# Kernel tuning notes

Hardware: AMD Instinct MI355X
Metric: run time of the kernel (lower is better)

## Reference

```python
import jax, jax.numpy as jnp
import numpy as np


def setup_inputs() -> dict:
    key = jax.random.key(0)
    k1, k2 = jax.random.split(key)
    B, N, F = 16, 4096, 512
    S, K = 8, 1024          # splits, symbols per codebook
    D = F // S              # sub-vector dim
    x = jax.random.normal(k1, (B, N, F), dtype=jnp.float32)
    # torch init: uniform(-1/symbols, 1/symbols)
    codebooks = jax.random.uniform(k2, (S, K, D), dtype=jnp.float32,
                                   minval=-1.0 / K, maxval=1.0 / K)
    return {"x": x, "codebooks": codebooks}


def reference(x, codebooks):
    B, N, F = x.shape
    S, K, D = codebooks.shape
    xs = x.reshape(B, N, S, D)                       # split into S chunks
    x2 = jnp.sum(xs * xs, axis=-1, keepdims=True)    # [B,N,S,1]
    c2 = jnp.sum(codebooks * codebooks, axis=-1)     # [S,K]
    xc = jnp.einsum('bnsd,skd->bnsk', xs, codebooks)
    dist = x2 + c2[None, None] - 2.0 * xc            # [B,N,S,K]
    idx = jnp.argmin(dist, axis=-1)                  # [B,N,S]
    # gather chosen code vectors per split -> [B,N,S,D]
    sym = codebooks[jnp.arange(S)[None, None, :], idx]
    sg = jax.lax.stop_gradient
    # straight-through quantized output
    quant = (xs + sg(sym - xs)).reshape(B, N, F)
    # per-split mse (mean over B,N,D of each chunk), summed over splits
    dev = (jnp.sum(jnp.mean((sym - sg(xs)) ** 2, axis=(0, 1, 3)))
           + 0.25 * jnp.sum(jnp.mean((xs - sg(sym)) ** 2, axis=(0, 1, 3))))
    return quant, dev
```

## Files before the change

### kernel.cpp

```cpp
#include <hip/hip_runtime.h>
#include <cstdint>

constexpr int Bv = 16, Nv = 4096, Fv = 512, Sv = 8, Kv = 1024, Dv = 64;
constexpr int Mv = Bv * Nv;
#define BDIM 256
constexpr int RG = 4;

using bf16x8 = __attribute__((ext_vector_type(8))) short;
using f32x4  = __attribute__((ext_vector_type(4))) float;
typedef unsigned short u16;
typedef unsigned int u32;

__device__ __forceinline__ u16 bf16rne(float f) {
  union { float f; u32 u; } v; v.f = f;
  u32 u = v.u + 0x7FFFu + ((v.u >> 16) & 1u);
  return (u16)(u >> 16);
}

__device__ __forceinline__ void gload_lds16(const void* g, void* lds) {
  __builtin_amdgcn_global_load_lds(
      (const __attribute__((address_space(1))) void*)g,
      (__attribute__((address_space(3))) void*)lds, 16, 0, 0);
}

__global__ void prep_kernel(const float* __restrict__ cb, u16* __restrict__ swz,
                            float* __restrict__ c2m) {
  int idx = blockIdx.x * BDIM + threadIdx.x;
  int cw = idx & (Kv - 1);
  const float4* src = (const float4*)(cb + (size_t)idx * Dv);
  float v[64];
  float s2 = 0.f;
#pragma unroll
  for (int i = 0; i < 16; ++i) {
    float4 f = src[i];
    v[i * 4 + 0] = f.x; v[i * 4 + 1] = f.y; v[i * 4 + 2] = f.z; v[i * 4 + 3] = f.w;
    s2 += f.x * f.x + f.y * f.y + f.z * f.z + f.w * f.w;
  }
  c2m[idx] = -0.5f * s2;
  uint4* out = (uint4*)(swz + (size_t)idx * Dv);
#pragma unroll
  for (int slot = 0; slot < 8; ++slot) {
    int slotp = slot ^ (cw & 7);
    u32 w[4];
#pragma unroll
    for (int p = 0; p < 4; ++p)
      w[p] = (u32)bf16rne(v[slot * 8 + p * 2]) | ((u32)bf16rne(v[slot * 8 + p * 2 + 1]) << 16);
    uint4 pk; pk.x = w[0]; pk.y = w[1]; pk.z = w[2]; pk.w = w[3];
    out[slotp] = pk;
  }
}

__global__ __launch_bounds__(BDIM, 4) void pq_mfma(
    const float* __restrict__ x, const float* __restrict__ cb,
    const u16* __restrict__ swz, const float* __restrict__ c2m_g,
    float* __restrict__ quant, float* __restrict__ devpart) {
  __shared__ __attribute__((aligned(16))) u16 ring[4][3][32 * Dv];
  __shared__ __attribute__((aligned(16))) float c2_lds[Kv];

  const int tid = threadIdx.x;
  const int s = blockIdx.y;
  const int row0 = blockIdx.x * 256;
  const int wave = tid >> 6, lane = tid & 63;
  const int l15 = lane & 15, lg = lane >> 4;
  const int slotp0 = lg ^ (l15 & 7);
  const int slotp1 = (4 + lg) ^ (l15 & 7);

  const u16* swz_s = swz + (size_t)s * Kv * Dv;

  auto stage = [&](int t, int slot) {
    const u16* src = swz_s + (size_t)t * (32 * Dv) + lane * 8;
    u16* dst = &ring[wave][slot][0];
#pragma unroll
    for (int it = 0; it < 4; ++it)
      gload_lds16(src + it * 512, dst + it * 512);
  };

  gload_lds16(c2m_g + s * Kv + tid * 4, &c2_lds[(tid & ~63) * 4]);
  stage(0, 0); stage(1, 1);

  bf16x8 xf[RG][2];
  float x2p[RG];
#pragma unroll
  for (int rg = 0; rg < RG; ++rg) {
    x2p[rg] = 0.f;
    const int row = row0 + wave * 64 + rg * 16 + l15;
    const float* xp = x + (size_t)row * Fv + s * Dv + lg * 8;
#pragma unroll
    for (int h = 0; h < 2; ++h) {
      float4 f0 = *(const float4*)(xp + h * 32);
      float4 f1 = *(const float4*)(xp + h * 32 + 4);
      x2p[rg] += f0.x * f0.x + f0.y * f0.y + f0.z * f0.z + f0.w * f0.w
               + f1.x * f1.x + f1.y * f1.y + f1.z * f1.z + f1.w * f1.w;
      bf16x8 v;
      v[0] = (short)bf16rne(f0.x); v[1] = (short)bf16rne(f0.y);
      v[2] = (short)bf16rne(f0.z); v[3] = (short)bf16rne(f0.w);
      v[4] = (short)bf16rne(f1.x); v[5] = (short)bf16rne(f1.y);
      v[6] = (short)bf16rne(f1.z); v[7] = (short)bf16rne(f1.w);
      xf[rg][h] = v;
    }
  }

  float bv[RG];
#pragma unroll
  for (int rg = 0; rg < RG; ++rg) bv[rg] = -3.0e38f;

  asm volatile("s_waitcnt vmcnt(8)" ::: "memory");
  __builtin_amdgcn_s_barrier();

  auto tile = [&](int t, int slot) {
    const u16* base = &ring[wave][slot][0];
    bf16x8 a00 = *(const bf16x8*)(base + l15 * Dv + slotp0 * 8);
    bf16x8 a01 = *(const bf16x8*)(base + l15 * Dv + slotp1 * 8);
    bf16x8 a10 = *(const bf16x8*)(base + (16 + l15) * Dv + slotp0 * 8);
    bf16x8 a11 = *(const bf16x8*)(base + (16 + l15) * Dv + slotp1 * 8);
    f32x4 c2v0 = *(const f32x4*)&c2_lds[t * 32 + lg * 4];
    f32x4 c2v1 = *(const f32x4*)&c2_lds[t * 32 + 16 + lg * 4];
    const u32 kb0 = (u32)(t * 32) | (u32)(lg * 4);
    const u32 kb1 = kb0 | 16u;
    __builtin_amdgcn_s_setprio(1);
#pragma unroll
    for (int rg = 0; rg < RG; ++rg) {
      f32x4 acc = __builtin_amdgcn_mfma_f32_16x16x32_bf16(a00, xf[rg][0], c2v0, 0, 0, 0);
      acc = __builtin_amdgcn_mfma_f32_16x16x32_bf16(a01, xf[rg][1], acc, 0, 0, 0);
      f32x4 acd = __builtin_amdgcn_mfma_f32_16x16x32_bf16(a10, xf[rg][0], c2v1, 0, 0, 0);
      acd = __builtin_amdgcn_mfma_f32_16x16x32_bf16(a11, xf[rg][1], acd, 0, 0, 0);
      float p0 = __builtin_bit_cast(float, __builtin_bit_cast(u32, acc[0]) | kb0);
      float p1 = __builtin_bit_cast(float, __builtin_bit_cast(u32, acc[1]) | (kb0 | 1u));
      float p2 = __builtin_bit_cast(float, __builtin_bit_cast(u32, acc[2]) | (kb0 | 2u));
      float p3 = __builtin_bit_cast(float, __builtin_bit_cast(u32, acc[3]) | (kb0 | 3u));
      float q0 = __builtin_bit_cast(float, __builtin_bit_cast(u32, acd[0]) | kb1);
      float q1 = __builtin_bit_cast(float, __builtin_bit_cast(u32, acd[1]) | (kb1 | 1u));
      float q2 = __builtin_bit_cast(float, __builtin_bit_cast(u32, acd[2]) | (kb1 | 2u));
      float q3 = __builtin_bit_cast(float, __builtin_bit_cast(u32, acd[3]) | (kb1 | 3u));
      float m0 = fmaxf(fmaxf(p0, p1), p2);
      float m1 = fmaxf(fmaxf(p3, q0), q1);
      float m2 = fmaxf(fmaxf(q2, q3), bv[rg]);
      bv[rg] = fmaxf(fmaxf(m0, m1), m2);
    }
    __builtin_amdgcn_s_setprio(0);
  };

#pragma unroll 1
  for (int b = 0; b < 30; b += 3) {
    stage(b + 2, 2);
    asm volatile("s_waitcnt vmcnt(8)" ::: "memory");
    tile(b, 0);
    stage(b + 3, 0);
    asm volatile("s_waitcnt vmcnt(8)" ::: "memory");
    tile(b + 1, 1);
    stage(b + 4, 1);
    asm volatile("s_waitcnt vmcnt(8)" ::: "memory");
    tile(b + 2, 2);
  }
  asm volatile("s_waitcnt vmcnt(4)" ::: "memory");
  tile(30, 0);
  asm volatile("s_waitcnt vmcnt(0)" ::: "memory");
  tile(31, 1);

#pragma unroll
  for (int rg = 0; rg < RG; ++rg) {
    float b = bv[rg], xx = x2p[rg];
    b = fmaxf(b, __shfl_xor(b, 16, 64)); xx += __shfl_xor(xx, 16, 64);
    b = fmaxf(b, __shfl_xor(b, 32, 64)); xx += __shfl_xor(xx, 32, 64);
    bv[rg] = b; x2p[rg] = xx;
  }

  float dev = 0.f;
#pragma unroll
  for (int rg = 0; rg < RG; ++rg) dev += x2p[rg] - 2.f * bv[rg];
#pragma unroll
  for (int m = 1; m <= 8; m <<= 1) dev += __shfl_xor(dev, m, 64);
  if (lane == 0)
    devpart[((size_t)blockIdx.y * gridDim.x + blockIdx.x) * 4 + wave] = dev;

  const float* cbs = cb + (size_t)s * Kv * Dv;
  float* qbase = quant + (size_t)(row0 + wave * 64) * Fv + s * Dv;
#pragma unroll
  for (int i = 0; i < 16; ++i) {
    int rl = i * 4 + lg;
    int kk = __shfl(__builtin_bit_cast(int, bv[i >> 2]), 4 * (i & 3) + lg, 64) & 1023;
    f32x4 v = *(const f32x4*)(cbs + (size_t)kk * Dv + l15 * 4);
    __builtin_nontemporal_store(v, (f32x4*)(qbase + (size_t)rl * Fv + l15 * 4));
  }
}

__global__ void dev_reduce(const float* __restrict__ part, float* __restrict__ out) {
  __shared__ float sred[256];
  int tid = threadIdx.x;
  float s = 0.f;
  for (int i = tid; i < 8192; i += 256) s += part[i];
  sred[tid] = s;
  __syncthreads();
  for (int off = 128; off > 0; off >>= 1) {
    if (tid < off) sred[tid] += sred[tid + off];
    __syncthreads();
  }
  if (tid == 0) out[0] = sred[0] * (1.25f / 4194304.0f);
}

extern "C" void kernel_launch(void* const* d_in, const int* in_sizes, int n_in,
                              void* d_out, int out_size, void* d_ws, size_t ws_size,
                              hipStream_t stream) {
  const float* x = (const float*)d_in[0];
  const float* cb = (const float*)d_in[1];
  float* quant = (float*)d_out;
  float* dev = quant + (size_t)Mv * Fv;

  u16* swz = (u16*)d_ws;
  float* c2m = (float*)(swz + (size_t)Sv * Kv * Dv);
  float* part = c2m + Sv * Kv;

  prep_kernel<<<(Sv * Kv) / BDIM, BDIM, 0, stream>>>(cb, swz, c2m);
  dim3 grid(Mv / 256, Sv);
  pq_mfma<<<grid, BDIM, 0, stream>>>(x, cb, swz, c2m, quant, part);
  dev_reduce<<<1, 256, 0, stream>>>(part, dev);
}
```

Baseline: 116.7 us.

## Shrink LDS ring to 16-code tiles with register double-buffered fragment reads

After: 126.1 us. 1.08x slower.

```diff
diff --git a/kernel.cpp b/kernel.cpp
--- a/kernel.cpp
+++ b/kernel.cpp
@@ -54,7 +54,7 @@
     const float* __restrict__ x, const float* __restrict__ cb,
     const u16* __restrict__ swz, const float* __restrict__ c2m_g,
     float* __restrict__ quant, float* __restrict__ devpart) {
-  __shared__ __attribute__((aligned(16))) u16 ring[4][3][32 * Dv];
+  __shared__ __attribute__((aligned(16))) u16 ring[4][2][16 * Dv];
   __shared__ __attribute__((aligned(16))) float c2_lds[Kv];
 
   const int tid = threadIdx.x;
@@ -66,17 +66,17 @@
   const int slotp1 = (4 + lg) ^ (l15 & 7);
 
   const u16* swz_s = swz + (size_t)s * Kv * Dv;
-
-  auto stage = [&](int t, int slot) {
-    const u16* src = swz_s + (size_t)t * (32 * Dv) + lane * 8;
-    u16* dst = &ring[wave][slot][0];
-#pragma unroll
-    for (int it = 0; it < 4; ++it)
-      gload_lds16(src + it * 512, dst + it * 512);
+  u16* slot0 = &ring[wave][0][0];
+  u16* slot1 = &ring[wave][1][0];
+
+  auto stage = [&](int t, u16* dst) {
+    const u16* src = swz_s + (size_t)t * (16 * Dv) + lane * 8;
+    gload_lds16(src, dst);
+    gload_lds16(src + 512, dst + 512);
   };
 
   gload_lds16(c2m_g + s * Kv + tid * 4, &c2_lds[(tid & ~63) * 4]);
-  stage(0, 0); stage(1, 1);
+  stage(0, slot0); stage(1, slot1);
 
   bf16x8 xf[RG][2];
   float x2p[RG];
@@ -104,58 +104,82 @@
 #pragma unroll
   for (int rg = 0; rg < RG; ++rg) bv[rg] = -3.0e38f;
 
-  asm volatile("s_waitcnt vmcnt(8)" ::: "memory");
+  asm volatile("s_waitcnt vmcnt(2)" ::: "memory");
   __builtin_amdgcn_s_barrier();
 
-  auto tile = [&](int t, int slot) {
-    const u16* base = &ring[wave][slot][0];
-    bf16x8 a00 = *(const bf16x8*)(base + l15 * Dv + slotp0 * 8);
-    bf16x8 a01 = *(const bf16x8*)(base + l15 * Dv + slotp1 * 8);
-    bf16x8 a10 = *(const bf16x8*)(base + (16 + l15) * Dv + slotp0 * 8);
-    bf16x8 a11 = *(const bf16x8*)(base + (16 + l15) * Dv + slotp1 * 8);
-    f32x4 c2v0 = *(const f32x4*)&c2_lds[t * 32 + lg * 4];
-    f32x4 c2v1 = *(const f32x4*)&c2_lds[t * 32 + 16 + lg * 4];
-    const u32 kb0 = (u32)(t * 32) | (u32)(lg * 4);
-    const u32 kb1 = kb0 | 16u;
+  const u16* r0s0 = slot0 + l15 * Dv + slotp0 * 8;
+  const u16* r1s0 = slot0 + l15 * Dv + slotp1 * 8;
+  const u16* r0s1 = slot1 + l15 * Dv + slotp0 * 8;
+  const u16* r1s1 = slot1 + l15 * Dv + slotp1 * 8;
+
+  bf16x8 aE0, aE1, aO0, aO1;
+  f32x4 c2E, c2O;
+
+  aE0 = *(const bf16x8*)r0s0;
+  aE1 = *(const bf16x8*)r1s0;
+  c2E = *(const f32x4*)&c2_lds[lg * 4];
+
+  auto readO = [&](int t1) {
+    aO0 = *(const bf16x8*)r0s1;
+    aO1 = *(const bf16x8*)r1s1;
+    c2O = *(const f32x4*)&c2_lds[t1 * 16 + lg * 4];
+  };
+  auto readE = [&](int t1) {
+    aE0 = *(const bf16x8*)r0s0;
+    aE1 = *(const bf16x8*)r1s0;
+    c2E = *(const f32x4*)&c2_lds[t1 * 16 + lg * 4];
+  };
+  auto computeE = [&](int t) {
+    const u32 kb = (u32)(t * 16) | (u32)(lg * 4);
     __builtin_amdgcn_s_setprio(1);
 #pragma unroll
     for (int rg = 0; rg < RG; ++rg) {
-      f32x4 acc = __builtin_amdgcn_mfma_f32_16x16x32_bf16(a00, xf[rg][0], c2v0, 0, 0, 0);
-      acc = __builtin_amdgcn_mfma_f32_16x16x32_bf16(a01, xf[rg][1], acc, 0, 0, 0);
-      f32x4 acd = __builtin_amdgcn_mfma_f32_16x16x32_bf16(a10, xf[rg][0], c2v1, 0, 0, 0);
-      acd = __builtin_amdgcn_mfma_f32_16x16x32_bf16(a11, xf[rg][1], acd, 0, 0, 0);
-      float p0 = __builtin_bit_cast(float, __builtin_bit_cast(u32, acc[0]) | kb0);
-      float p1 = __builtin_bit_cast(float, __builtin_bit_cast(u32, acc[1]) | (kb0 | 1u));
-      float p2 = __builtin_bit_cast(float, __builtin_bit_cast(u32, acc[2]) | (kb0 | 2u));
-      float p3 = __builtin_bit_cast(float, __builtin_bit_cast(u32, acc[3]) | (kb0 | 3u));
-      float q0 = __builtin_bit_cast(float, __builtin_bit_cast(u32, acd[0]) | kb1);
-      float q1 = __builtin_bit_cast(float, __builtin_bit_cast(u32, acd[1]) | (kb1 | 1u));
-      float q2 = __builtin_bit_cast(float, __builtin_bit_cast(u32, acd[2]) | (kb1 | 2u));
-      float q3 = __builtin_bit_cast(float, __builtin_bit_cast(u32, acd[3]) | (kb1 | 3u));
-      float m0 = fmaxf(fmaxf(p0, p1), p2);
-      float m1 = fmaxf(fmaxf(p3, q0), q1);
-      float m2 = fmaxf(fmaxf(q2, q3), bv[rg]);
-      bv[rg] = fmaxf(fmaxf(m0, m1), m2);
+      f32x4 acc = __builtin_amdgcn_mfma_f32_16x16x32_bf16(aE0, xf[rg][0], c2E, 0, 0, 0);
+      acc = __builtin_amdgcn_mfma_f32_16x16x32_bf16(aE1, xf[rg][1], acc, 0, 0, 0);
+      float p0 = __builtin_bit_cast(float, __builtin_bit_cast(u32, acc[0]) | kb);
+      float p1 = __builtin_bit_cast(float, __builtin_bit_cast(u32, acc[1]) | (kb | 1u));
+      float p2 = __builtin_bit_cast(float, __builtin_bit_cast(u32, acc[2]) | (kb | 2u));
+      float p3 = __builtin_bit_cast(float, __builtin_bit_cast(u32, acc[3]) | (kb | 3u));
+      bv[rg] = fmaxf(fmaxf(fmaxf(p0, p1), fmaxf(p2, p3)), bv[rg]);
     }
     __builtin_amdgcn_s_setprio(0);
   };
+  auto computeO = [&](int t) {
+    const u32 kb = (u32)(t * 16) | (u32)(lg * 4);
+    __builtin_amdgcn_s_setprio(1);
+#pragma unroll
+    for (int rg = 0; rg < RG; ++rg) {
+      f32x4 acc = __builtin_amdgcn_mfma_f32_16x16x32_bf16(aO0, xf[rg][0], c2O, 0, 0, 0);
+      acc = __builtin_amdgcn_mfma_f32_16x16x32_bf16(aO1, xf[rg][1], acc, 0, 0, 0);
+      float p0 = __builtin_bit_cast(float, __builtin_bit_cast(u32, acc[0]) | kb);
+      float p1 = __builtin_bit_cast(float, __builtin_bit_cast(u32, acc[1]) | (kb | 1u));
+      float p2 = __builtin_bit_cast(float, __builtin_bit_cast(u32, acc[2]) | (kb | 2u));
+      float p3 = __builtin_bit_cast(float, __builtin_bit_cast(u32, acc[3]) | (kb | 3u));
+      bv[rg] = fmaxf(fmaxf(fmaxf(p0, p1), fmaxf(p2, p3)), bv[rg]);
+    }
+    __builtin_amdgcn_s_setprio(0);
+  };
 
 #pragma unroll 1
-  for (int b = 0; b < 30; b += 3) {
-    stage(b + 2, 2);
-    asm volatile("s_waitcnt vmcnt(8)" ::: "memory");
-    tile(b, 0);
-    stage(b + 3, 0);
-    asm volatile("s_waitcnt vmcnt(8)" ::: "memory");
-    tile(b + 1, 1);
-    stage(b + 4, 1);
-    asm volatile("s_waitcnt vmcnt(8)" ::: "memory");
-    tile(b + 2, 2);
-  }
-  asm volatile("s_waitcnt vmcnt(4)" ::: "memory");
-  tile(30, 0);
+  for (int t = 0; t < 60; t += 2) {
+    stage(t + 2, slot0);
+    asm volatile("s_waitcnt vmcnt(2)" ::: "memory");
+    readO(t + 1);
+    computeE(t);
+    stage(t + 3, slot1);
+    asm volatile("s_waitcnt vmcnt(2)" ::: "memory");
+    readE(t + 2);
+    computeO(t + 1);
+  }
+  stage(62, slot0);
+  asm volatile("s_waitcnt vmcnt(2)" ::: "memory");
+  readO(61); computeE(60);
+  stage(63, slot1);
+  asm volatile("s_waitcnt vmcnt(2)" ::: "memory");
+  readE(62); computeO(61);
   asm volatile("s_waitcnt vmcnt(0)" ::: "memory");
-  tile(31, 1);
+  readO(63); computeE(62);
+  computeO(63);
 
 #pragma unroll
   for (int rg = 0; rg < RG; ++rg) {
```
